# Performance work log

Measured on AMD Instinct MI355X. Metric: run time of the kernel, lower is better.

Reference implementation:

```python
import jax, jax.numpy as jnp
import numpy as np

B, DM, DC, H = 16384, 1024, 8, 256  # batch, MRI feat dim, clinical feat dim, hidden_dim


def setup_inputs() -> dict:
    key = jax.random.key(0)
    ks = jax.random.split(key, 16)
    f = lambda k, s: jax.random.normal(k, s, dtype=jnp.float32)
    return {
        # encoder outputs (4 MRI modalities @1024-d, clinical @8-d)
        'feat_t1': f(ks[0], (B, DM)), 'feat_t1c': f(ks[1], (B, DM)),
        'feat_t2': f(ks[2], (B, DM)), 'feat_flair': f(ks[3], (B, DM)),
        'feat_cl': f(ks[4], (B, DC)),
        # per-modality projection Linears (MRI ones stacked: same math as 4 separate Linears)
        'Wp_mri': f(ks[5], (4, H, DM)) * 0.02, 'bp_mri': jnp.zeros((4, H), jnp.float32),
        'Wp_cl': f(ks[6], (H, DC)) * 0.02, 'bp_cl': jnp.zeros((H,), jnp.float32),
        # attention MLP: Linear(256,64) -> Tanh -> Linear(64,1)
        'Wa1': f(ks[7], (64, H)) * 0.02, 'ba1': jnp.zeros((64,), jnp.float32),
        'Wa2': f(ks[8], (1, 64)) * 0.02, 'ba2': jnp.zeros((1,), jnp.float32),
        # classifier: 256->128 LN ReLU -> 128->64 LN ReLU -> 64->1 (num_class-1)
        'Wc1': f(ks[9], (128, H)) * 0.02, 'bc1': jnp.zeros((128,), jnp.float32),
        'g1': jnp.ones((128,), jnp.float32), 'be1': jnp.zeros((128,), jnp.float32),
        'Wc2': f(ks[10], (64, 128)) * 0.02, 'bc2': jnp.zeros((64,), jnp.float32),
        'g2': jnp.ones((64,), jnp.float32), 'be2': jnp.zeros((64,), jnp.float32),
        'Wc3': f(ks[11], (1, 64)) * 0.02, 'bc3': jnp.zeros((1,), jnp.float32),
    }


def _ln(x, g, b, eps=1e-5):
    m = jnp.mean(x, axis=-1, keepdims=True)
    v = jnp.var(x, axis=-1, keepdims=True)
    return (x - m) * jax.lax.rsqrt(v + eps) * g + b


def reference(feat_t1, feat_t1c, feat_t2, feat_flair, feat_cl,
              Wp_mri, bp_mri, Wp_cl, bp_cl,
              Wa1, ba1, Wa2, ba2,
              Wc1, bc1, g1, be1, Wc2, bc2, g2, be2, Wc3, bc3):
    mri = jnp.stack([feat_t1, feat_t1c, feat_t2, feat_flair], axis=1)  # [B,4,DM]
    pm = jnp.einsum('bmd,mhd->bmh', mri, Wp_mri) + bp_mri              # [B,4,H] per-modality Linear
    pc = feat_cl @ Wp_cl.T + bp_cl                                     # [B,H]
    proj = jnp.concatenate([pm, pc[:, None, :]], axis=1)               # [B,5,H] == torch.stack(proj_feats, dim=1)
    scores = jnp.tanh(proj @ Wa1.T + ba1) @ Wa2.T + ba2                # [B,5,1]
    attn_weights = jax.nn.softmax(scores, axis=1)                      # softmax over modalities
    fused = jnp.sum(attn_weights * proj, axis=1)                       # [B,H]
    h = jax.nn.relu(_ln(fused @ Wc1.T + bc1, g1, be1))                 # dropout is identity in eval
    h = jax.nn.relu(_ln(h @ Wc2.T + bc2, g2, be2))
    out = h @ Wc3.T + bc3                                              # [B,1]
    return out, attn_weights
```

## Files before the change

kernel.cpp:

```cpp
#include <hip/hip_runtime.h>
#include <math.h>

typedef unsigned short u16;
typedef unsigned int   u32;
typedef __bf16 bf16x8 __attribute__((ext_vector_type(8)));
typedef float  f32x4  __attribute__((ext_vector_type(4)));
typedef u16    u16x8  __attribute__((ext_vector_type(8)));
typedef u16    u16x4  __attribute__((ext_vector_type(4)));

#define B_TOT 16384
#define DM_   1024
#define H_    256

#define WS_SCORES 41943040
#define WS_WP     42270720
#define WS_WA1    44367872
#define WS_WC1    44400640
#define WS_WC2    44466176

__device__ __forceinline__ u16 f2bf(float f){
  __bf16 h = (__bf16)f;
  return __builtin_bit_cast(u16, h);
}
__device__ __forceinline__ float bf2f(u16 h){
  return __builtin_bit_cast(float, ((u32)h) << 16);
}
__device__ __forceinline__ u16x4 cvt4(f32x4 a){
  u16x4 h;
  #pragma unroll
  for (int j = 0; j < 4; j++) h[j] = f2bf(a[j]);
  return h;
}
__device__ __forceinline__ f32x4 mfma16(bf16x8 a, bf16x8 b, f32x4 c){
  return __builtin_amdgcn_mfma_f32_16x16x32_bf16(a, b, c, 0, 0, 0);
}

__global__ void k0_convert(const float* __restrict__ s0, u16* __restrict__ d0, int n0,
                           const float* __restrict__ s1, u16* __restrict__ d1, int n1,
                           const float* __restrict__ s2, u16* __restrict__ d2, int n2,
                           const float* __restrict__ s3, u16* __restrict__ d3, int n3)
{
  int total4 = (n0 + n1 + n2 + n3) >> 2;
  for (int i = blockIdx.x * blockDim.x + threadIdx.x; i < total4; i += gridDim.x * blockDim.x){
    int e = i << 2;
    const float* s; u16* d; int off;
    if (e < n0)            { s = s0; d = d0; off = e; }
    else if (e < n0+n1)    { s = s1; d = d1; off = e - n0; }
    else if (e < n0+n1+n2) { s = s2; d = d2; off = e - n0 - n1; }
    else                   { s = s3; d = d3; off = e - n0 - n1 - n2; }
    f32x4 f = *(const f32x4*)(s + off);
    *(u16x4*)(d + off) = cvt4(f);
  }
}

__global__ __launch_bounds__(256) void k1b_clin(
    const float* __restrict__ fcl, const float* __restrict__ Wpcl, const float* __restrict__ bpcl,
    const u16* __restrict__ Wa1bf, const float* __restrict__ ba1,
    const float* __restrict__ Wa2, const float* __restrict__ ba2,
    u16* __restrict__ proj, float* __restrict__ scores)
{
  __shared__ u16 pcs[4][16*264];
  const int tid = threadIdx.x, lane = tid & 63, wv = tid >> 6;
  const int l15 = lane & 15, l4 = lane >> 4;
  const int rbase = blockIdx.x * 64 + wv * 16;

  f32x4 wA[4], wB[4];
  f32x4 bp = *(const f32x4*)(bpcl + lane * 4);
  #pragma unroll
  for (int c = 0; c < 4; c++){
    wA[c] = *(const f32x4*)(Wpcl + (lane*4 + c) * 8);
    wB[c] = *(const f32x4*)(Wpcl + (lane*4 + c) * 8 + 4);
  }
  #pragma unroll 4
  for (int r = 0; r < 16; r++){
    int row = rbase + r;
    f32x4 fA = *(const f32x4*)(fcl + (size_t)row * 8);
    f32x4 fB = *(const f32x4*)(fcl + (size_t)row * 8 + 4);
    u16x4 h;
    #pragma unroll
    for (int c = 0; c < 4; c++){
      float v = bp[c] + fA[0]*wA[c][0] + fA[1]*wA[c][1] + fA[2]*wA[c][2] + fA[3]*wA[c][3]
                      + fB[0]*wB[c][0] + fB[1]*wB[c][1] + fB[2]*wB[c][2] + fB[3]*wB[c][3];
      h[c] = f2bf(v);
    }
    *(u16x4*)(proj + (size_t)row * 1280 + 1024 + lane * 4) = h;
    *(u16x4*)(&pcs[wv][r * 264 + lane * 4]) = h;
  }
  f32x4 at[4];
  #pragma unroll
  for (int nf = 0; nf < 4; nf++) at[nf] = f32x4{0.f,0.f,0.f,0.f};
  #pragma unroll
  for (int kk = 0; kk < 8; kk++){
    bf16x8 a = *(const bf16x8*)((const char*)&pcs[wv][0] + l15*528 + kk*64 + l4*16);
    #pragma unroll
    for (int nf = 0; nf < 4; nf++){
      bf16x8 b = *(const bf16x8*)((const char*)Wa1bf + (nf*16 + l15)*512 + kk*64 + l4*16);
      at[nf] = mfma16(a, b, at[nf]);
    }
  }
  float po[4] = {0.f,0.f,0.f,0.f};
  #pragma unroll
  for (int nf = 0; nf < 4; nf++){
    int col = nf*16 + l15;
    float bb = ba1[col], w2 = Wa2[col];
    #pragma unroll
    for (int rg = 0; rg < 4; rg++) po[rg] += tanhf(at[nf][rg] + bb) * w2;
  }
  #pragma unroll
  for (int rg = 0; rg < 4; rg++){
    #pragma unroll
    for (int d = 1; d < 16; d <<= 1) po[rg] += __shfl_xor(po[rg], d);
  }
  if (l15 == 0){
    float b2 = ba2[0];
    #pragma unroll
    for (int rg = 0; rg < 4; rg++)
      scores[(size_t)(rbase + l4*4 + rg) * 5 + 4] = po[rg] + b2;
  }
}

__global__ __launch_bounds__(512, 4) void k1_proj(
    const float* __restrict__ ft1, const float* __restrict__ ft1c,
    const float* __restrict__ ft2, const float* __restrict__ ftfl,
    const u16* __restrict__ Wpbf, const float* __restrict__ bpm,
    const u16* __restrict__ Wa1bf, const float* __restrict__ ba1,
    const float* __restrict__ Wa2, const float* __restrict__ ba2,
    u16* __restrict__ proj, float* __restrict__ scores)
{
  extern __shared__ char lds[];
  const int l  = blockIdx.x;
  const int mm = (l & 7) >> 1;
  const int bx = ((l >> 3) << 1) | (l & 1);
  const int b0 = bx * 128;
  const int tid = threadIdx.x;
  const int lane = tid & 63;
  const int wv = tid >> 6;
  const int wm = wv >> 2, wn = wv & 3;
  const int l15 = lane & 15, l4 = lane >> 4;

  const float* Am = (mm == 0) ? ft1 : ((mm == 1) ? ft1c : ((mm == 2) ? ft2 : ftfl));
  const u16*   Wm = Wpbf + (size_t)mm * (H_ * DM_);

  const int ar  = tid >> 4;
  const int ac4 = tid & 15;

  f32x4 acc[4][4];
  #pragma unroll
  for (int i = 0; i < 4; i++)
    #pragma unroll
    for (int j = 0; j < 4; j++) acc[i][j] = f32x4{0.f,0.f,0.f,0.f};

  #pragma unroll
  for (int i = 0; i < 4; i++){
    int r = ar + 32*i;
    f32x4 a = *(const f32x4*)(Am + (size_t)(b0 + r) * DM_ + ac4 * 4);
    *(u16x4*)(lds + r*128 + ((ac4*8) ^ ((r & 7) << 4))) = cvt4(a);
  }
  #pragma unroll
  for (int i = 0; i < 4; i++){
    int q = i*512 + tid; int r = q >> 3, c = q & 7;
    u16x8 w = *(const u16x8*)(Wm + (size_t)r * DM_ + c * 8);
    *(u16x8*)(lds + 16384 + r*128 + ((c*16) ^ ((r & 7) << 4))) = w;
  }
  __syncthreads();

  for (int kt = 0; kt < 16; ++kt){
    f32x4 aR[4]; u16x8 wR[4];
    if (kt < 15){
      #pragma unroll
      for (int i = 0; i < 4; i++){
        int r = ar + 32*i;
        aR[i] = *(const f32x4*)(Am + (size_t)(b0 + r) * DM_ + (kt+1)*64 + ac4*4);
      }
      #pragma unroll
      for (int i = 0; i < 4; i++){
        int q = i*512 + tid; int r = q >> 3, c = q & 7;
        wR[i] = *(const u16x8*)(Wm + (size_t)r * DM_ + (kt+1)*64 + c*8);
      }
    }
    #pragma unroll
    for (int kk = 0; kk < 2; kk++){
      int kb = kk*64 + l4*16;
      bf16x8 af[4];
      #pragma unroll
      for (int mf = 0; mf < 4; mf++){
        int r = wm*64 + mf*16 + l15;
        af[mf] = *(const bf16x8*)(lds + r*128 + (kb ^ ((r & 7) << 4)));
      }
      #pragma unroll
      for (int nf = 0; nf < 4; nf++){
        int r = wn*64 + nf*16 + l15;
        bf16x8 bfr = *(const bf16x8*)(lds + 16384 + r*128 + (kb ^ ((r & 7) << 4)));
        #pragma unroll
        for (int mf = 0; mf < 4; mf++)
          acc[mf][nf] = mfma16(af[mf], bfr, acc[mf][nf]);
      }
    }
    __syncthreads();
    if (kt < 15){
      #pragma unroll
      for (int i = 0; i < 4; i++){
        int r = ar + 32*i;
        *(u16x4*)(lds + r*128 + ((ac4*8) ^ ((r & 7) << 4))) = cvt4(aR[i]);
      }
      #pragma unroll
      for (int i = 0; i < 4; i++){
        int q = i*512 + tid; int r = q >> 3, c = q & 7;
        *(u16x8*)(lds + 16384 + r*128 + ((c*16) ^ ((r & 7) << 4))) = wR[i];
      }
      __syncthreads();
    }
  }

  {
    float bias[4];
    #pragma unroll
    for (int nf = 0; nf < 4; nf++) bias[nf] = bpm[mm*256 + wn*64 + nf*16 + l15];
    #pragma unroll
    for (int mf = 0; mf < 4; mf++){
      #pragma unroll
      for (int nf = 0; nf < 4; nf++){
        int cc = wn*64 + nf*16 + l15;
        #pragma unroll
        for (int rg = 0; rg < 4; rg++){
          int r = wm*64 + mf*16 + l4*4 + rg;
          *(u16*)(lds + r*512 + ((cc*2) ^ ((r & 7) << 4))) = f2bf(acc[mf][nf][rg] + bias[nf]);
        }
      }
    }
  }
  __syncthreads();

  #pragma unroll
  for (int i = 0; i < 8; i++){
    int q = i*512 + tid;
    int r = q >> 5, c = q & 31;
    u16x8 v = *(const u16x8*)(lds + r*512 + ((c*16) ^ ((r & 7) << 4)));
    *(u16x8*)((char*)proj + (size_t)(b0 + r) * 2560 + mm*512 + c*16) = v;
  }
  {
    f32x4 a2[4];
    #pragma unroll
    for (int nf = 0; nf < 4; nf++) a2[nf] = f32x4{0.f,0.f,0.f,0.f};
    #pragma unroll
    for (int kk = 0; kk < 8; kk++){
      int kb = kk*64 + l4*16;
      int r = wv*16 + l15;
      bf16x8 af = *(const bf16x8*)(lds + r*512 + (kb ^ ((r & 7) << 4)));
      #pragma unroll
      for (int nf = 0; nf < 4; nf++){
        int n = nf*16 + l15;
        bf16x8 bfr = *(const bf16x8*)((const char*)Wa1bf + n*512 + kb);
        a2[nf] = mfma16(af, bfr, a2[nf]);
      }
    }
    float p0 = 0.f, p1 = 0.f, p2 = 0.f, p3 = 0.f;
    #pragma unroll
    for (int nf = 0; nf < 4; nf++){
      int n = nf*16 + l15;
      float w2 = Wa2[n], bn = ba1[n];
      p0 += tanhf(a2[nf][0] + bn) * w2;
      p1 += tanhf(a2[nf][1] + bn) * w2;
      p2 += tanhf(a2[nf][2] + bn) * w2;
      p3 += tanhf(a2[nf][3] + bn) * w2;
    }
    #pragma unroll
    for (int d = 1; d < 16; d <<= 1){
      p0 += __shfl_xor(p0, d); p1 += __shfl_xor(p1, d);
      p2 += __shfl_xor(p2, d); p3 += __shfl_xor(p3, d);
    }
    if (l15 == 0){
      float bav = ba2[0];
      int rb = wv*16 + l4*4;
      scores[(size_t)(b0 + rb + 0)*5 + mm] = p0 + bav;
      scores[(size_t)(b0 + rb + 1)*5 + mm] = p1 + bav;
      scores[(size_t)(b0 + rb + 2)*5 + mm] = p2 + bav;
      scores[(size_t)(b0 + rb + 3)*5 + mm] = p3 + bav;
    }
  }
}

__global__ __launch_bounds__(256) void k2_cls(
    const u16* __restrict__ proj, const float* __restrict__ scores,
    const u16* __restrict__ Wc1bf, const u16* __restrict__ Wc2bf,
    const float* __restrict__ bc1, const float* __restrict__ g1, const float* __restrict__ be1,
    const float* __restrict__ bc2, const float* __restrict__ g2, const float* __restrict__ be2,
    const float* __restrict__ Wc3, const float* __restrict__ bc3,
    float* __restrict__ outp)
{
  __shared__ u16 h1s[4][16*136];
  const int tid = threadIdx.x, lane = tid & 63, wv = tid >> 6;
  const int l15 = lane & 15, l4 = lane >> 4;
  const int b0 = blockIdx.x * 64;
  const int rowA = b0 + wv*16 + l15;

  const float* sc = scores + (size_t)rowA * 5;
  float s0 = sc[0], s1 = sc[1], s2 = sc[2], s3 = sc[3], s4 = sc[4];
  float mx = fmaxf(fmaxf(fmaxf(s0, s1), fmaxf(s2, s3)), s4);
  float e0 = expf(s0-mx), e1 = expf(s1-mx), e2 = expf(s2-mx), e3 = expf(s3-mx), e4 = expf(s4-mx);
  float inv = 1.0f / (e0 + e1 + e2 + e3 + e4);
  float w0 = e0*inv, w1 = e1*inv, w2 = e2*inv, w3 = e3*inv, w4 = e4*inv;
  if (l4 == 0){
    float* ap = outp + B_TOT + (size_t)rowA * 5;
    ap[0] = w0; ap[1] = w1; ap[2] = w2; ap[3] = w3; ap[4] = w4;
  }

  bf16x8 af[8];
  const u16* pr = proj + (size_t)rowA * 1280 + l4*8;
  #pragma unroll
  for (int kk = 0; kk < 8; kk++){
    u16x8 p0v = *(const u16x8*)(pr + kk*32);
    u16x8 p1v = *(const u16x8*)(pr + 256  + kk*32);
    u16x8 p2v = *(const u16x8*)(pr + 512  + kk*32);
    u16x8 p3v = *(const u16x8*)(pr + 768  + kk*32);
    u16x8 p4v = *(const u16x8*)(pr + 1024 + kk*32);
    bf16x8 a;
    #pragma unroll
    for (int j = 0; j < 8; j++)
      a[j] = (__bf16)(w0*bf2f(p0v[j]) + w1*bf2f(p1v[j]) + w2*bf2f(p2v[j])
                    + w3*bf2f(p3v[j]) + w4*bf2f(p4v[j]));
    af[kk] = a;
  }

  f32x4 acc1[8];
  #pragma unroll
  for (int of = 0; of < 8; of++) acc1[of] = f32x4{0.f,0.f,0.f,0.f};
  #pragma unroll
  for (int kk = 0; kk < 8; kk++){
    #pragma unroll
    for (int of = 0; of < 8; of++){
      bf16x8 b = *(const bf16x8*)((const char*)Wc1bf + (of*16 + l15)*512 + kk*64 + l4*16);
      acc1[of] = mfma16(af[kk], b, acc1[of]);
    }
  }
  float sum1[4] = {0.f,0.f,0.f,0.f};
  #pragma unroll
  for (int of = 0; of < 8; of++){
    float bb = bc1[of*16 + l15];
    #pragma unroll
    for (int rg = 0; rg < 4; rg++){ acc1[of][rg] += bb; sum1[rg] += acc1[of][rg]; }
  }
  #pragma unroll
  for (int rg = 0; rg < 4; rg++){
    #pragma unroll
    for (int d = 1; d < 16; d <<= 1) sum1[rg] += __shfl_xor(sum1[rg], d);
  }
  float vs1[4] = {0.f,0.f,0.f,0.f};
  float mean1[4];
  #pragma unroll
  for (int rg = 0; rg < 4; rg++) mean1[rg] = sum1[rg] * 0.0078125f;
  #pragma unroll
  for (int of = 0; of < 8; of++)
    #pragma unroll
    for (int rg = 0; rg < 4; rg++){ float dd = acc1[of][rg] - mean1[rg]; vs1[rg] += dd*dd; }
  #pragma unroll
  for (int rg = 0; rg < 4; rg++){
    #pragma unroll
    for (int d = 1; d < 16; d <<= 1) vs1[rg] += __shfl_xor(vs1[rg], d);
  }
  float is1[4];
  #pragma unroll
  for (int rg = 0; rg < 4; rg++) is1[rg] = rsqrtf(vs1[rg] * 0.0078125f + 1e-5f);
  #pragma unroll
  for (int of = 0; of < 8; of++){
    int col = of*16 + l15;
    float gg = g1[col], bb = be1[col];
    #pragma unroll
    for (int rg = 0; rg < 4; rg++){
      float h = fmaxf((acc1[of][rg] - mean1[rg]) * is1[rg] * gg + bb, 0.f);
      h1s[wv][(l4*4 + rg)*136 + col] = f2bf(h);
    }
  }

  f32x4 acc2[4];
  #pragma unroll
  for (int of = 0; of < 4; of++) acc2[of] = f32x4{0.f,0.f,0.f,0.f};
  #pragma unroll
  for (int kk = 0; kk < 4; kk++){
    bf16x8 a2 = *(const bf16x8*)((const char*)&h1s[wv][0] + l15*272 + kk*64 + l4*16);
    #pragma unroll
    for (int of = 0; of < 4; of++){
      bf16x8 b = *(const bf16x8*)((const char*)Wc2bf + (of*16 + l15)*256 + kk*64 + l4*16);
      acc2[of] = mfma16(a2, b, acc2[of]);
    }
  }
  float sum2[4] = {0.f,0.f,0.f,0.f};
  #pragma unroll
  for (int of = 0; of < 4; of++){
    float bb = bc2[of*16 + l15];
    #pragma unroll
    for (int rg = 0; rg < 4; rg++){ acc2[of][rg] += bb; sum2[rg] += acc2[of][rg]; }
  }
  #pragma unroll
  for (int rg = 0; rg < 4; rg++){
    #pragma unroll
    for (int d = 1; d < 16; d <<= 1) sum2[rg] += __shfl_xor(sum2[rg], d);
  }
  float mean2[4], vs2[4] = {0.f,0.f,0.f,0.f};
  #pragma unroll
  for (int rg = 0; rg < 4; rg++) mean2[rg] = sum2[rg] * 0.015625f;
  #pragma unroll
  for (int of = 0; of < 4; of++)
    #pragma unroll
    for (int rg = 0; rg < 4; rg++){ float dd = acc2[of][rg] - mean2[rg]; vs2[rg] += dd*dd; }
  #pragma unroll
  for (int rg = 0; rg < 4; rg++){
    #pragma unroll
    for (int d = 1; d < 16; d <<= 1) vs2[rg] += __shfl_xor(vs2[rg], d);
  }
  float po[4] = {0.f,0.f,0.f,0.f};
  #pragma unroll
  for (int of = 0; of < 4; of++){
    int col = of*16 + l15;
    float gg = g2[col], bb = be2[col], w3c = Wc3[col];
    #pragma unroll
    for (int rg = 0; rg < 4; rg++){
      float is2 = rsqrtf(vs2[rg] * 0.015625f + 1e-5f);
      float h = fmaxf((acc2[of][rg] - mean2[rg]) * is2 * gg + bb, 0.f);
      po[rg] += h * w3c;
    }
  }
  #pragma unroll
  for (int rg = 0; rg < 4; rg++){
    #pragma unroll
    for (int d = 1; d < 16; d <<= 1) po[rg] += __shfl_xor(po[rg], d);
  }
  if (l15 == 0){
    float b3 = bc3[0];
    #pragma unroll
    for (int rg = 0; rg < 4; rg++)
      outp[b0 + wv*16 + l4*4 + rg] = po[rg] + b3;
  }
}

extern "C" void kernel_launch(void* const* d_in, const int* in_sizes, int n_in,
                              void* d_out, int out_size, void* d_ws, size_t ws_size,
                              hipStream_t stream)
{
  (void)in_sizes; (void)n_in; (void)out_size; (void)ws_size;
  const float* ft1  = (const float*)d_in[0];
  const float* ft1c = (const float*)d_in[1];
  const float* ft2  = (const float*)d_in[2];
  const float* ftfl = (const float*)d_in[3];
  const float* fcl  = (const float*)d_in[4];
  const float* Wpmri= (const float*)d_in[5];
  const float* bpm  = (const float*)d_in[6];
  const float* Wpcl = (const float*)d_in[7];
  const float* bpcl = (const float*)d_in[8];
  const float* Wa1  = (const float*)d_in[9];
  const float* ba1  = (const float*)d_in[10];
  const float* Wa2  = (const float*)d_in[11];
  const float* ba2  = (const float*)d_in[12];
  const float* Wc1  = (const float*)d_in[13];
  const float* bc1  = (const float*)d_in[14];
  const float* g1   = (const float*)d_in[15];
  const float* be1  = (const float*)d_in[16];
  const float* Wc2  = (const float*)d_in[17];
  const float* bc2  = (const float*)d_in[18];
  const float* g2   = (const float*)d_in[19];
  const float* be2  = (const float*)d_in[20];
  const float* Wc3  = (const float*)d_in[21];
  const float* bc3  = (const float*)d_in[22];
  float* outp = (float*)d_out;
  char* ws = (char*)d_ws;

  u16*   proj   = (u16*)(ws);
  float* scores = (float*)(ws + WS_SCORES);
  u16*   Wpbf   = (u16*)(ws + WS_WP);
  u16*   Wa1bf  = (u16*)(ws + WS_WA1);
  u16*   Wc1bf  = (u16*)(ws + WS_WC1);
  u16*   Wc2bf  = (u16*)(ws + WS_WC2);

  (void)hipFuncSetAttribute((const void*)k1_proj, hipFuncAttributeMaxDynamicSharedMemorySize, 65536);

  k0_convert<<<dim3(512), dim3(256), 0, stream>>>(
      Wpmri, Wpbf, 4 * H_ * DM_,
      Wa1,  Wa1bf, 64 * H_,
      Wc1,  Wc1bf, 128 * H_,
      Wc2,  Wc2bf, 64 * 128);

  k1b_clin<<<dim3(256), dim3(256), 0, stream>>>(
      fcl, Wpcl, bpcl, Wa1bf, ba1, Wa2, ba2, proj, scores);

  k1_proj<<<dim3(512), dim3(512), 65536, stream>>>(
      ft1, ft1c, ft2, ftfl, Wpbf, bpm, Wa1bf, ba1, Wa2, ba2, proj, scores);

  k2_cls<<<dim3(256), dim3(256), 0, stream>>>(
      proj, scores, Wc1bf, Wc2bf, bc1, g1, be1, bc2, g2, be2, Wc3, bc3, outp);
}
```

Measured before the change: 123.6 us.

## Use direct global-to-LDS async loads with double buffering and smaller M tiles in projection

The projection GEMM now loads fp32 activations and bf16 weights straight into LDS with global_load_lds, double-buffered, so the next K tile streams in while the current one is computed. Activations are kept as fp32 in LDS and converted to bf16 at fragment load. The M tile is halved from 128 to 64 rows, with twice as many blocks, less LDS per block and a higher occupancy hint. The aim is to remove register staging and one barrier per K step and to improve latency hiding. In exchange the per-block reuse of weights is smaller and only half the waves do the attention-score epilogue.

```diff
diff --git a/kernel.cpp b/kernel.cpp
--- a/kernel.cpp
+++ b/kernel.cpp
@@ -33,6 +33,11 @@
 }
 __device__ __forceinline__ f32x4 mfma16(bf16x8 a, bf16x8 b, f32x4 c){
   return __builtin_amdgcn_mfma_f32_16x16x32_bf16(a, b, c, 0, 0, 0);
+}
+__device__ __forceinline__ void glds16(const void* g, void* l){
+  __builtin_amdgcn_global_load_lds(
+      (const __attribute__((address_space(1))) void*)g,
+      (__attribute__((address_space(3))) void*)l, 16, 0, 0);
 }
 
 __global__ void k0_convert(const float* __restrict__ s0, u16* __restrict__ d0, int n0,
@@ -119,7 +124,7 @@
   }
 }
 
-__global__ __launch_bounds__(512, 4) void k1_proj(
+__global__ __launch_bounds__(512, 6) void k1_proj(
     const float* __restrict__ ft1, const float* __restrict__ ft1c,
     const float* __restrict__ ft2, const float* __restrict__ ftfl,
     const u16* __restrict__ Wpbf, const float* __restrict__ bpm,
@@ -128,10 +133,10 @@
     u16* __restrict__ proj, float* __restrict__ scores)
 {
   extern __shared__ char lds[];
-  const int l  = blockIdx.x;
-  const int mm = (l & 7) >> 1;
-  const int bx = ((l >> 3) << 1) | (l & 1);
-  const int b0 = bx * 128;
+  const int bid = blockIdx.x;
+  const int mm = (bid & 7) >> 1;
+  const int bx = ((bid >> 3) << 1) | (bid & 1);
+  const int b0 = bx * 64;
   const int tid = threadIdx.x;
   const int lane = tid & 63;
   const int wv = tid >> 6;
@@ -139,77 +144,81 @@
   const int l15 = lane & 15, l4 = lane >> 4;
 
   const float* Am = (mm == 0) ? ft1 : ((mm == 1) ? ft1c : ((mm == 2) ? ft2 : ftfl));
-  const u16*   Wm = Wpbf + (size_t)mm * (H_ * DM_);
-
-  const int ar  = tid >> 4;
-  const int ac4 = tid & 15;
-
-  f32x4 acc[4][4];
-  #pragma unroll
-  for (int i = 0; i < 4; i++)
+  const char*  Wm = (const char*)(Wpbf + (size_t)mm * (H_ * DM_));
+  const char*  Ab8 = (const char*)Am;
+
+  const int a_r = tid >> 3, a_c = tid & 7;
+  const size_t a_src0 = (size_t)(b0 + a_r) * 4096 + (size_t)((a_c*16) ^ ((a_r & 7) << 4));
+  const int a_dstw = (tid >> 6) * 1024;
+  int w_pr[2], w_c[2]; size_t w_src0[2];
+  #pragma unroll
+  for (int i = 0; i < 2; i++){
+    int q = i*512 + tid; w_pr[i] = q >> 3; w_c[i] = q & 7;
+    int zp = (w_c[i]*16) ^ ((w_pr[i] & 7) << 4);
+    int col = 2*w_pr[i] + (zp >> 6);
+    w_src0[i] = (size_t)col * 2048 + (size_t)(zp & 63);
+  }
+
+  f32x4 acc[2][4];
+  #pragma unroll
+  for (int i = 0; i < 2; i++)
     #pragma unroll
     for (int j = 0; j < 4; j++) acc[i][j] = f32x4{0.f,0.f,0.f,0.f};
 
-  #pragma unroll
-  for (int i = 0; i < 4; i++){
-    int r = ar + 32*i;
-    f32x4 a = *(const f32x4*)(Am + (size_t)(b0 + r) * DM_ + ac4 * 4);
-    *(u16x4*)(lds + r*128 + ((ac4*8) ^ ((r & 7) << 4))) = cvt4(a);
-  }
-  #pragma unroll
-  for (int i = 0; i < 4; i++){
-    int q = i*512 + tid; int r = q >> 3, c = q & 7;
-    u16x8 w = *(const u16x8*)(Wm + (size_t)r * DM_ + c * 8);
-    *(u16x8*)(lds + 16384 + r*128 + ((c*16) ^ ((r & 7) << 4))) = w;
-  }
+  int a_off[2], w_off[4];
+  #pragma unroll
+  for (int mf = 0; mf < 2; mf++){
+    int r = wm*32 + mf*16 + l15;
+    a_off[mf] = r*128 + ((l4*32) ^ ((r & 7) << 4));
+  }
+  int a_off2[2];
+  #pragma unroll
+  for (int mf = 0; mf < 2; mf++){
+    int r = wm*32 + mf*16 + l15;
+    a_off2[mf] = r*128 + (((l4*32) + 16) ^ ((r & 7) << 4));
+  }
+  #pragma unroll
+  for (int nf = 0; nf < 4; nf++){
+    int col = wn*64 + nf*16 + l15;
+    int p = col >> 1, qq = col & 1;
+    w_off[nf] = p*128 + (((qq*64) + l4*16) ^ ((p & 7) << 4));
+  }
+
+  glds16(Ab8 + a_src0, lds + a_dstw);
+  #pragma unroll
+  for (int i = 0; i < 2; i++)
+    glds16(Wm + w_src0[i], lds + 16384 + i*8192 + a_dstw);
   __syncthreads();
 
-  for (int kt = 0; kt < 16; ++kt){
-    f32x4 aR[4]; u16x8 wR[4];
-    if (kt < 15){
+  for (int kt = 0; kt < 32; ++kt){
+    const int cur = kt & 1;
+    if (kt < 31){
+      const int nb = cur ^ 1;
+      glds16(Ab8 + a_src0 + (size_t)(kt+1)*128, lds + nb*8192 + a_dstw);
       #pragma unroll
-      for (int i = 0; i < 4; i++){
-        int r = ar + 32*i;
-        aR[i] = *(const f32x4*)(Am + (size_t)(b0 + r) * DM_ + (kt+1)*64 + ac4*4);
-      }
+      for (int i = 0; i < 2; i++)
+        glds16(Wm + w_src0[i] + (size_t)(kt+1)*64, lds + 16384 + nb*16384 + i*8192 + a_dstw);
+    }
+    const char* Abuf = lds + cur*8192;
+    const char* Wbuf = lds + 16384 + cur*16384;
+    bf16x8 af[2];
+    #pragma unroll
+    for (int mf = 0; mf < 2; mf++){
+      f32x4 a0 = *(const f32x4*)(Abuf + a_off[mf]);
+      f32x4 a1 = *(const f32x4*)(Abuf + a_off2[mf]);
+      bf16x8 h;
       #pragma unroll
-      for (int i = 0; i < 4; i++){
-        int q = i*512 + tid; int r = q >> 3, c = q & 7;
-        wR[i] = *(const u16x8*)(Wm + (size_t)r * DM_ + (kt+1)*64 + c*8);
-      }
-    }
-    #pragma unroll
-    for (int kk = 0; kk < 2; kk++){
-      int kb = kk*64 + l4*16;
-      bf16x8 af[4];
+      for (int j = 0; j < 4; j++){ h[j] = (__bf16)a0[j]; h[4+j] = (__bf16)a1[j]; }
+      af[mf] = h;
+    }
+    #pragma unroll
+    for (int nf = 0; nf < 4; nf++){
+      bf16x8 wfr = *(const bf16x8*)(Wbuf + w_off[nf]);
       #pragma unroll
-      for (int mf = 0; mf < 4; mf++){
-        int r = wm*64 + mf*16 + l15;
-        af[mf] = *(const bf16x8*)(lds + r*128 + (kb ^ ((r & 7) << 4)));
-      }
-      #pragma unroll
-      for (int nf = 0; nf < 4; nf++){
-        int r = wn*64 + nf*16 + l15;
-        bf16x8 bfr = *(const bf16x8*)(lds + 16384 + r*128 + (kb ^ ((r & 7) << 4)));
-        #pragma unroll
-        for (int mf = 0; mf < 4; mf++)
-          acc[mf][nf] = mfma16(af[mf], bfr, acc[mf][nf]);
-      }
+      for (int mf = 0; mf < 2; mf++)
+        acc[mf][nf] = mfma16(af[mf], wfr, acc[mf][nf]);
     }
     __syncthreads();
-    if (kt < 15){
-      #pragma unroll
-      for (int i = 0; i < 4; i++){
-        int r = ar + 32*i;
-        *(u16x4*)(lds + r*128 + ((ac4*8) ^ ((r & 7) << 4))) = cvt4(aR[i]);
-      }
-      #pragma unroll
-      for (int i = 0; i < 4; i++){
-        int q = i*512 + tid; int r = q >> 3, c = q & 7;
-        *(u16x8*)(lds + 16384 + r*128 + ((c*16) ^ ((r & 7) << 4))) = wR[i];
-      }
-      __syncthreads();
-    }
   }
 
   {
@@ -217,13 +226,13 @@
     #pragma unroll
     for (int nf = 0; nf < 4; nf++) bias[nf] = bpm[mm*256 + wn*64 + nf*16 + l15];
     #pragma unroll
-    for (int mf = 0; mf < 4; mf++){
+    for (int mf = 0; mf < 2; mf++){
       #pragma unroll
       for (int nf = 0; nf < 4; nf++){
         int cc = wn*64 + nf*16 + l15;
         #pragma unroll
         for (int rg = 0; rg < 4; rg++){
-          int r = wm*64 + mf*16 + l4*4 + rg;
+          int r = wm*32 + mf*16 + l4*4 + rg;
           *(u16*)(lds + r*512 + ((cc*2) ^ ((r & 7) << 4))) = f2bf(acc[mf][nf][rg] + bias[nf]);
         }
       }
@@ -232,13 +241,13 @@
   __syncthreads();
 
   #pragma unroll
-  for (int i = 0; i < 8; i++){
+  for (int i = 0; i < 4; i++){
     int q = i*512 + tid;
     int r = q >> 5, c = q & 31;
     u16x8 v = *(const u16x8*)(lds + r*512 + ((c*16) ^ ((r & 7) << 4)));
     *(u16x8*)((char*)proj + (size_t)(b0 + r) * 2560 + mm*512 + c*16) = v;
   }
-  {
+  if (wv < 4){
     f32x4 a2[4];
     #pragma unroll
     for (int nf = 0; nf < 4; nf++) a2[nf] = f32x4{0.f,0.f,0.f,0.f};
@@ -246,12 +255,12 @@
     for (int kk = 0; kk < 8; kk++){
       int kb = kk*64 + l4*16;
       int r = wv*16 + l15;
-      bf16x8 af = *(const bf16x8*)(lds + r*512 + (kb ^ ((r & 7) << 4)));
+      bf16x8 afr = *(const bf16x8*)(lds + r*512 + (kb ^ ((r & 7) << 4)));
       #pragma unroll
       for (int nf = 0; nf < 4; nf++){
         int n = nf*16 + l15;
         bf16x8 bfr = *(const bf16x8*)((const char*)Wa1bf + n*512 + kb);
-        a2[nf] = mfma16(af, bfr, a2[nf]);
+        a2[nf] = mfma16(afr, bfr, a2[nf]);
       }
     }
     float p0 = 0.f, p1 = 0.f, p2 = 0.f, p3 = 0.f;
@@ -471,8 +480,6 @@
   u16*   Wc1bf  = (u16*)(ws + WS_WC1);
   u16*   Wc2bf  = (u16*)(ws + WS_WC2);
 
-  (void)hipFuncSetAttribute((const void*)k1_proj, hipFuncAttributeMaxDynamicSharedMemorySize, 65536);
-
   k0_convert<<<dim3(512), dim3(256), 0, stream>>>(
       Wpmri, Wpbf, 4 * H_ * DM_,
       Wa1,  Wa1bf, 64 * H_,
@@ -482,7 +489,7 @@
   k1b_clin<<<dim3(256), dim3(256), 0, stream>>>(
       fcl, Wpcl, bpcl, Wa1bf, ba1, Wa2, ba2, proj, scores);
 
-  k1_proj<<<dim3(512), dim3(512), 65536, stream>>>(
+  k1_proj<<<dim3(1024), dim3(512), 49152, stream>>>(
       ft1, ft1c, ft2, ftfl, Wpbf, bpm, Wa1bf, ba1, Wa2, ba2, proj, scores);
 
   k2_cls<<<dim3(256), dim3(256), 0, stream>>>(
```

Result: slower. 149.3 us (+20.8%).
